# Optimization experiments

Hardware: AMD Instinct MI355X
Metric: run time of the kernel (lower is better)

Reference implementation:

```python
import jax, jax.numpy as jnp
import numpy as np

NX = NY = NZ = 256   # linear_freqs
D1 = D2 = D3 = 8     # reduced_freqs
DF = 16              # feature_dim
NPTS = 131072


def softplus_b10(x):
    # torch F.softplus(x, beta=10, threshold=1)
    bx = 10.0 * x
    return jnp.where(bx > 1.0, x, 0.1 * jnp.log1p(jnp.exp(jnp.minimum(bx, 30.0))))


def grid_sample2d(vol, gx, gy):
    """Bilinear grid_sample, align_corners=True. vol:[C,H,W] (complex ok),
    gx,gy:[N] in [-1,1] (gx indexes W, gy indexes H). Returns [C,N]."""
    C, H, W = vol.shape
    ix = (gx + 1.0) * 0.5 * (W - 1)
    iy = (gy + 1.0) * 0.5 * (H - 1)
    x0f = jnp.floor(ix)
    y0f = jnp.floor(iy)
    wx = ix - x0f
    wy = iy - y0f
    x0 = jnp.clip(x0f.astype(jnp.int32), 0, W - 1)
    x1 = jnp.clip(x0 + 1, 0, W - 1)
    y0 = jnp.clip(y0f.astype(jnp.int32), 0, H - 1)
    y1 = jnp.clip(y0 + 1, 0, H - 1)
    v00 = vol[:, y0, x0]
    v01 = vol[:, y0, x1]
    v10 = vol[:, y1, x0]
    v11 = vol[:, y1, x1]
    return (v00 * (1 - wy) * (1 - wx) + v01 * (1 - wy) * wx
            + v10 * wy * (1 - wx) + v11 * wy * wx)


def batch_irfft(ph, x, ff, T):
    """ph:[D,d,N] complex, x:[N] in [-1,1], ff:[d] freqs. Returns [D,N]."""
    xx = (x + 1.0) * 0.5 * (T - 1) / T                    # [N]
    ang = 2.0 * np.pi * xx[:, None] * ff[None, :]         # [N,d]
    scale = jnp.where(ff > 0, 2.0, 1.0)
    tw_re = jnp.cos(ang) * scale
    tw_im = jnp.sin(ang) * scale
    return (jnp.einsum('dfn,nf->dn', ph.real, tw_re)
            - jnp.einsum('dfn,nf->dn', ph.imag, tw_im))


def setup_inputs() -> dict:
    key = jax.random.key(0)
    ks = jax.random.split(key, 8)
    inputs = jax.random.uniform(ks[0], (NPTS, 3), jnp.float32, minval=-1.0, maxval=1.0)
    s = 0.01
    Fx_re = jax.random.normal(ks[1], (1, DF, D1, NY, NZ), jnp.float32) * s
    Fx_im = jax.random.normal(ks[2], (1, DF, D1, NY, NZ), jnp.float32) * s
    Fy_re = jax.random.normal(ks[3], (1, DF, NX, D2, NZ), jnp.float32) * s
    Fy_im = jax.random.normal(ks[4], (1, DF, NX, D2, NZ), jnp.float32) * s
    Fz_re = jax.random.normal(ks[5], (1, DF, NX, NY, D3), jnp.float32) * s
    Fz_im = jax.random.normal(ks[6], (1, DF, NX, NY, D3), jnp.float32) * s
    alpha_params = jnp.array([0.001], jnp.float32)
    return {"inputs": inputs, "Fx_re": Fx_re, "Fx_im": Fx_im,
            "Fy_re": Fy_re, "Fy_im": Fy_im, "Fz_re": Fz_re, "Fz_im": Fz_im,
            "alpha_params": alpha_params}


def reference(inputs, Fx_re, Fx_im, Fy_re, Fy_im, Fz_re, Fz_im, alpha_params):
    alpha = softplus_b10(alpha_params)[0]
    Fx = (Fx_re + 1j * Fx_im) * alpha        # [1,D,d1,Ny,Nz]
    Fy = (Fy_re + 1j * Fy_im) * alpha        # [1,D,Nx,d2,Nz]
    Fz = (Fz_re + 1j * Fz_im) * alpha        # [1,D,Nx,Ny,d3]
    # inverse FFT over the two full (linear) spectral axes
    Fx = jnp.fft.ifftn(Fx, axes=(3, 4), norm='forward')
    Fy = jnp.fft.ifftn(Fy, axes=(2, 4), norm='forward')
    Fz = jnp.fft.ifftn(Fz, axes=(2, 3), norm='forward')
    xs, ys, zs = inputs[:, 0], inputs[:, 1], inputs[:, 2]
    N = inputs.shape[0]
    kx = jnp.arange(D1, dtype=jnp.float32)   # linear sampling axis [0,1,...]
    ky = jnp.arange(D2, dtype=jnp.float32)
    kz = jnp.arange(D3, dtype=jnp.float32)
    # complex bilinear gathers (H,W) = (Ny,Nz) / (Nx,Nz) / (Ny,Nx)
    fx = grid_sample2d(Fx.reshape(DF * D1, NY, NZ), zs, ys).reshape(DF, D1, N)
    fy = grid_sample2d(jnp.transpose(Fy, (0, 1, 3, 2, 4)).reshape(DF * D2, NX, NZ),
                       zs, xs).reshape(DF, D2, N)
    fz = grid_sample2d(jnp.transpose(Fz, (0, 1, 4, 3, 2)).reshape(DF * D3, NY, NX),
                       xs, ys).reshape(DF, D3, N)
    fxx = batch_irfft(fx, xs, kx, NX)
    fyy = batch_irfft(fy, ys, ky, NY)
    fzz = batch_irfft(fz, zs, kz, NZ)
    return (fxx + fyy + fzz).T               # [N, DF]
```

## Files before the change

kernel.cpp:

```cpp
#include <hip/hip_runtime.h>
#include <hip/hip_fp16.h>
#include <math.h>

#define NPTS 131072
#define RS 264

__device__ __forceinline__ float dev_alpha(const float* __restrict__ ap) {
    float x = ap[0];
    float bx = 10.0f * x;
    if (bx > 1.0f) return x;
    float e = expf(fminf(bx, 30.0f));
    return 0.1f * log1pf(e);
}

__device__ __forceinline__ void fft16_reg(float* re, float* im) {
    #define SW(a,b) { float t=re[a]; re[a]=re[b]; re[b]=t; t=im[a]; im[a]=im[b]; im[b]=t; }
    SW(1,8) SW(2,4) SW(3,12) SW(5,10) SW(7,14) SW(11,13)
    #undef SW
    const float C[8] = {1.f, 0.9238795325112867f, 0.7071067811865476f, 0.3826834323650898f,
                        0.f, -0.3826834323650898f, -0.7071067811865476f, -0.9238795325112867f};
    const float S[8] = {0.f, 0.3826834323650898f, 0.7071067811865476f, 0.9238795325112867f,
                        1.f, 0.9238795325112867f, 0.7071067811865476f, 0.3826834323650898f};
    #pragma unroll
    for (int m = 1; m < 16; m <<= 1) {
        #pragma unroll
        for (int k = 0; k < 16; k += 2 * m) {
            #pragma unroll
            for (int j = 0; j < m; ++j) {
                float wc = C[j * (8 / m)], ws = S[j * (8 / m)];
                int i0 = k + j, i1 = i0 + m;
                float tr = re[i1] * wc - im[i1] * ws;
                float ti = re[i1] * ws + im[i1] * wc;
                re[i1] = re[i0] - tr; im[i1] = im[i0] - ti;
                re[i0] += tr;         im[i0] += ti;
            }
        }
    }
}

__device__ __forceinline__ void fft256_block(float* lre, float* lim, int tid) {
    const int r = tid >> 4, s = tid & 15;
    float xr[16], xi[16];
    #pragma unroll
    for (int a = 0; a < 16; ++a) {
        xr[a] = lre[r * RS + 16 * a + s];
        xi[a] = lim[r * RS + 16 * a + s];
    }
    __syncthreads();
    fft16_reg(xr, xi);
    #pragma unroll
    for (int c = 0; c < 16; ++c) {
        float sn, cs;
        __sincosf(0.0245436926061703f * (float)(s * c), &sn, &cs);
        float tr = xr[c] * cs - xi[c] * sn;
        float ti = xr[c] * sn + xi[c] * cs;
        int idx = r * RS + 16 * c + (s ^ c);
        lre[idx] = tr; lim[idx] = ti;
    }
    __syncthreads();
    #pragma unroll
    for (int b = 0; b < 16; ++b) {
        int idx = r * RS + 16 * s + (b ^ s);
        xr[b] = lre[idx]; xi[b] = lim[idx];
    }
    __syncthreads();
    fft16_reg(xr, xi);
    #pragma unroll
    for (int d = 0; d < 16; ++d) {
        int idx = r * RS + 16 * d + s;
        lre[idx] = xr[d]; lim[idx] = xi[d];
    }
    __syncthreads();
}

__device__ __forceinline__ unsigned packh2(float re, float im) {
    return __builtin_bit_cast(unsigned, __floats2half2_rn(re, im));
}

__global__ __launch_bounds__(256) void fft_pass1_xy(
    const float4* __restrict__ Fre4, const float4* __restrict__ Fim4,
    const float* __restrict__ alpha_p, uint4* __restrict__ GT4,
    int Sd4, int Sa4)
{
    __shared__ float lre[16 * RS], lim[16 * RS];
    const int tid = threadIdx.x, bg = blockIdx.x;
    const int d = bg & 7, ag = (bg >> 3) & 15, f = bg >> 7;
    const int a0 = ag * 16, c = f * 8 + d;
    const int base4 = f * 131072 + d * Sd4 + a0 * Sa4;
    const float alpha = dev_alpha(alpha_p);
    #pragma unroll
    for (int j = 0; j < 4; ++j) {
        int i4 = tid + 256 * j;
        int ar = i4 >> 6, b4 = i4 & 63;
        float4 vr = Fre4[base4 + ar * Sa4 + b4];
        float4 vi = Fim4[base4 + ar * Sa4 + b4];
        int o = ar * RS + 4 * b4;
        lre[o+0]=vr.x*alpha; lre[o+1]=vr.y*alpha; lre[o+2]=vr.z*alpha; lre[o+3]=vr.w*alpha;
        lim[o+0]=vi.x*alpha; lim[o+1]=vi.y*alpha; lim[o+2]=vi.z*alpha; lim[o+3]=vi.w*alpha;
    }
    __syncthreads();
    fft256_block(lre, lim, tid);
    const int g = tid >> 2, rq = tid & 3;
    #pragma unroll
    for (int j = 0; j < 4; ++j) {
        int k = g + 64 * j;
        uint4 ov;
        ov.x = packh2(lre[(4*rq+0)*RS+k], lim[(4*rq+0)*RS+k]);
        ov.y = packh2(lre[(4*rq+1)*RS+k], lim[(4*rq+1)*RS+k]);
        ov.z = packh2(lre[(4*rq+2)*RS+k], lim[(4*rq+2)*RS+k]);
        ov.w = packh2(lre[(4*rq+3)*RS+k], lim[(4*rq+3)*RS+k]);
        GT4[((c * 256 + k) * 256 + a0) / 4 + rq] = ov;
    }
}

__global__ __launch_bounds__(256) void fft_pass2_xy(
    const uint4* __restrict__ GT4, uint4* __restrict__ V4)
{
    __shared__ float lre[16 * RS], lim[16 * RS];
    const int tid = threadIdx.x, bg = blockIdx.x;
    const int cg = bg & 7, b = bg >> 3, c0 = cg * 16;
    #pragma unroll
    for (int j = 0; j < 4; ++j) {
        int i4 = tid + 256 * j;
        int cr = i4 >> 6, a4 = i4 & 63;
        uint4 gv = GT4[(((c0 + cr) * 256 + b) * 256) / 4 + a4];
        int o = cr * RS + 4 * a4;
        float2 e;
        e = __half22float2(__builtin_bit_cast(__half2, gv.x)); lre[o+0]=e.x; lim[o+0]=e.y;
        e = __half22float2(__builtin_bit_cast(__half2, gv.y)); lre[o+1]=e.x; lim[o+1]=e.y;
        e = __half22float2(__builtin_bit_cast(__half2, gv.z)); lre[o+2]=e.x; lim[o+2]=e.y;
        e = __half22float2(__builtin_bit_cast(__half2, gv.w)); lre[o+3]=e.x; lim[o+3]=e.y;
    }
    __syncthreads();
    fft256_block(lre, lim, tid);
    const int g = tid >> 2, cq = tid & 3;
    #pragma unroll
    for (int j = 0; j < 4; ++j) {
        int k = g + 64 * j;
        uint4 ov;
        ov.x = packh2(lre[(4*cq+0)*RS+k], lim[(4*cq+0)*RS+k]);
        ov.y = packh2(lre[(4*cq+1)*RS+k], lim[(4*cq+1)*RS+k]);
        ov.z = packh2(lre[(4*cq+2)*RS+k], lim[(4*cq+2)*RS+k]);
        ov.w = packh2(lre[(4*cq+3)*RS+k], lim[(4*cq+3)*RS+k]);
        V4[((b * 256 + k) * 128 + c0) / 4 + cq] = ov;
    }
}

__global__ __launch_bounds__(256) void fft_pass1_z(
    const float4* __restrict__ Fre4, const float4* __restrict__ Fim4,
    const float* __restrict__ alpha_p, uint4* __restrict__ GTz4)
{
    __shared__ float lre[16 * RS], lim[16 * RS];
    const int tid = threadIdx.x, bg = blockIdx.x;
    const int f = bg >> 7, kxp = bg & 127;
    const int base4 = f * 131072 + kxp * 1024;
    const float alpha = dev_alpha(alpha_p);
    #pragma unroll
    for (int j = 0; j < 4; ++j) {
        int i4 = tid + 256 * j;
        int kxo = i4 >> 9, ky = (i4 & 511) >> 1, t0 = i4 & 1;
        float4 vr = Fre4[base4 + i4];
        float4 vi = Fim4[base4 + i4];
        int row = kxo * 8 + 4 * t0;
        lre[(row+0)*RS + ky] = vr.x*alpha; lim[(row+0)*RS + ky] = vi.x*alpha;
        lre[(row+1)*RS + ky] = vr.y*alpha; lim[(row+1)*RS + ky] = vi.y*alpha;
        lre[(row+2)*RS + ky] = vr.z*alpha; lim[(row+2)*RS + ky] = vi.z*alpha;
        lre[(row+3)*RS + ky] = vr.w*alpha; lim[(row+3)*RS + ky] = vi.w*alpha;
    }
    __syncthreads();
    fft256_block(lre, lim, tid);
    const int g = tid >> 2, rq = tid & 3;
    #pragma unroll
    for (int j = 0; j < 4; ++j) {
        int k = g + 64 * j;
        uint4 ov;
        ov.x = packh2(lre[(4*rq+0)*RS+k], lim[(4*rq+0)*RS+k]);
        ov.y = packh2(lre[(4*rq+1)*RS+k], lim[(4*rq+1)*RS+k]);
        ov.z = packh2(lre[(4*rq+2)*RS+k], lim[(4*rq+2)*RS+k]);
        ov.w = packh2(lre[(4*rq+3)*RS+k], lim[(4*rq+3)*RS+k]);
        GTz4[k * 8192 + f * 512 + kxp * 4 + rq] = ov;
    }
}

__global__ __launch_bounds__(256) void fft_pass2_z(
    const uint4* __restrict__ GTz4, uint4* __restrict__ V4)
{
    __shared__ float lre[16 * RS], lim[16 * RS];
    const int tid = threadIdx.x, bg = blockIdx.x;
    const int fp = bg & 7, b = bg >> 3;
    const int base4 = b * 8192 + fp * 1024;
    #pragma unroll
    for (int j = 0; j < 4; ++j) {
        int i4 = tid + 256 * j;
        int fo = i4 >> 9, kx = (i4 & 511) >> 1, t0 = i4 & 1;
        uint4 gv = GTz4[base4 + i4];
        int row = fo * 8 + 4 * t0;
        float2 e;
        e = __half22float2(__builtin_bit_cast(__half2, gv.x)); lre[(row+0)*RS+kx]=e.x; lim[(row+0)*RS+kx]=e.y;
        e = __half22float2(__builtin_bit_cast(__half2, gv.y)); lre[(row+1)*RS+kx]=e.x; lim[(row+1)*RS+kx]=e.y;
        e = __half22float2(__builtin_bit_cast(__half2, gv.z)); lre[(row+2)*RS+kx]=e.x; lim[(row+2)*RS+kx]=e.y;
        e = __half22float2(__builtin_bit_cast(__half2, gv.w)); lre[(row+3)*RS+kx]=e.x; lim[(row+3)*RS+kx]=e.y;
    }
    __syncthreads();
    fft256_block(lre, lim, tid);
    const int g = tid >> 2, rq = tid & 3;
    #pragma unroll
    for (int j = 0; j < 4; ++j) {
        int k = g + 64 * j;
        uint4 ov;
        ov.x = packh2(lre[(4*rq+0)*RS+k], lim[(4*rq+0)*RS+k]);
        ov.y = packh2(lre[(4*rq+1)*RS+k], lim[(4*rq+1)*RS+k]);
        ov.z = packh2(lre[(4*rq+2)*RS+k], lim[(4*rq+2)*RS+k]);
        ov.w = packh2(lre[(4*rq+3)*RS+k], lim[(4*rq+3)*RS+k]);
        V4[(b * 256 + k) * 32 + fp * 4 + rq] = ov;
    }
}

__device__ __forceinline__ int bin8(float v) {
    return min(max((int)((v + 1.0f) * 127.5f), 0), 255);
}
__global__ __launch_bounds__(256) void zero_hist(unsigned* __restrict__ h) {
    h[blockIdx.x * 256 + threadIdx.x] = 0;
}
__global__ __launch_bounds__(256) void hist_k(const float* __restrict__ pts, unsigned* __restrict__ h) {
    int pid = blockIdx.x * 256 + threadIdx.x;
    int key = bin8(pts[pid * 3 + 2]) * 256 + bin8(pts[pid * 3 + 1]);
    atomicAdd(&h[key], 1u);
}
__global__ __launch_bounds__(256) void scan_k(const unsigned* __restrict__ h, unsigned* __restrict__ cur) {
    __shared__ unsigned part[256];
    const int t = threadIdx.x;
    unsigned sum = 0;
    for (int i = 0; i < 256; ++i) sum += h[t * 256 + i];
    part[t] = sum;
    __syncthreads();
    for (int o = 1; o < 256; o <<= 1) {
        unsigned v = part[t];
        unsigned add = (t >= o) ? part[t - o] : 0u;
        __syncthreads();
        part[t] = v + add;
        __syncthreads();
    }
    unsigned run = (t > 0) ? part[t - 1] : 0u;
    for (int i = 0; i < 256; ++i) {
        cur[t * 256 + i] = run;
        run += h[t * 256 + i];
    }
}
__global__ __launch_bounds__(256) void scatter_k(const float* __restrict__ pts,
                                                 unsigned* __restrict__ cur,
                                                 float4* __restrict__ ptsS) {
    int pid = blockIdx.x * 256 + threadIdx.x;
    float x = pts[pid * 3 + 0], y = pts[pid * 3 + 1], z = pts[pid * 3 + 2];
    int key = bin8(z) * 256 + bin8(y);
    unsigned pos = atomicAdd(&cur[key], 1u);
    ptsS[pos] = make_float4(x, y, z, __uint_as_float((unsigned)pid));
}

__device__ __forceinline__ float4 bsample(const uint2* __restrict__ V,
                                          float gx, float gy, bool swap, int lane) {
    float ix = (gx + 1.0f) * 127.5f;
    float iy = (gy + 1.0f) * 127.5f;
    float x0f = floorf(ix), y0f = floorf(iy);
    float wx = ix - x0f, wy = iy - y0f;
    int x0 = min(max((int)x0f, 0), 255);
    int x1 = min(x0 + 1, 255);
    int y0 = min(max((int)y0f, 0), 255);
    int y1 = min(y0 + 1, 255);
    int rA, rB, rC, rD;
    if (swap) { rA = y0*256+x0; rB = y0*256+x1; rC = y1*256+x0; rD = y1*256+x1; }
    else      { rA = x0*256+y0; rB = x1*256+y0; rC = x0*256+y1; rD = x1*256+y1; }
    uint2 a = V[rA * 64 + lane];
    uint2 b = V[rB * 64 + lane];
    uint2 c = V[rC * 64 + lane];
    uint2 d = V[rD * 64 + lane];
    __half2 w00 = __float2half2_rn((1.0f - wy) * (1.0f - wx));
    __half2 w01 = __float2half2_rn((1.0f - wy) * wx);
    __half2 w10 = __float2half2_rn(wy * (1.0f - wx));
    __half2 w11 = __float2half2_rn(wy * wx);
    __half2 acc0 = __hmul2(w00, __builtin_bit_cast(__half2, a.x));
    __half2 acc1 = __hmul2(w00, __builtin_bit_cast(__half2, a.y));
    acc0 = __hfma2(w01, __builtin_bit_cast(__half2, b.x), acc0);
    acc1 = __hfma2(w01, __builtin_bit_cast(__half2, b.y), acc1);
    acc0 = __hfma2(w10, __builtin_bit_cast(__half2, c.x), acc0);
    acc1 = __hfma2(w10, __builtin_bit_cast(__half2, c.y), acc1);
    acc0 = __hfma2(w11, __builtin_bit_cast(__half2, d.x), acc0);
    acc1 = __hfma2(w11, __builtin_bit_cast(__half2, d.y), acc1);
    return make_float4(__low2float(acc0), __high2float(acc0),
                       __low2float(acc1), __high2float(acc1));
}

__device__ __forceinline__ float irdft(float4 s, float tw, int lane) {
    const float TWO_PI = 6.28318530717958647692f;
    float xx = (tw + 1.0f) * 0.5f * (255.0f / 256.0f);
    int k0 = (lane & 3) * 2;
    float sa, ca, sb, cb;
    __sincosf(TWO_PI * xx * (float)k0,       &sa, &ca);
    __sincosf(TWO_PI * xx * (float)(k0 + 1), &sb, &cb);
    float sc0 = (k0 > 0) ? 2.0f : 1.0f;
    return sc0 * (s.x * ca - s.y * sa) + 2.0f * (s.z * cb - s.w * sb);
}

__global__ __launch_bounds__(256) void sample_all(
    const uint2* __restrict__ Vx, const uint2* __restrict__ Vy, const uint2* __restrict__ Vz,
    const float4* __restrict__ ptsS, float* __restrict__ out)
{
    const int lb = blockIdx.x;
    const int chunk = (lb & 7) * 4096 + (lb >> 3);
    const int wid = chunk * 4 + ((int)threadIdx.x >> 6);
    const int lane = threadIdx.x & 63;
    float4 p = ptsS[wid];
    const float xs = p.x, ys = p.y, zs = p.z;
    const int pid = (int)__float_as_uint(p.w);

    float4 sx = bsample(Vx, zs, ys, false, lane);
    float4 sy = bsample(Vy, zs, xs, false, lane);
    float4 sz = bsample(Vz, xs, ys, true, lane);

    float pv = irdft(sx, xs, lane) + irdft(sy, ys, lane) + irdft(sz, zs, lane);
    pv += __shfl_xor(pv, 1, 64);
    pv += __shfl_xor(pv, 2, 64);
    if ((lane & 3) == 0) out[pid * 16 + (lane >> 2)] = pv;
}

extern "C" void kernel_launch(void* const* d_in, const int* in_sizes, int n_in,
                              void* d_out, int out_size, void* d_ws, size_t ws_size,
                              hipStream_t stream) {
    const float* pts     = (const float*)d_in[0];
    const float* Fx_re   = (const float*)d_in[1];
    const float* Fx_im   = (const float*)d_in[2];
    const float* Fy_re   = (const float*)d_in[3];
    const float* Fy_im   = (const float*)d_in[4];
    const float* Fz_re   = (const float*)d_in[5];
    const float* Fz_im   = (const float*)d_in[6];
    const float* alpha_p = (const float*)d_in[7];
    float* out = (float*)d_out;

    char* ws = (char*)d_ws;
    const size_t MB = 1024 * 1024;
    uint4* Vx4 = (uint4*)(ws);
    uint4* Vy4 = (uint4*)(ws + 32 * MB);
    uint4* Vz4 = (uint4*)(ws + 64 * MB);
    uint4* GT4 = (uint4*)(ws + 96 * MB);
    unsigned* hist = (unsigned*)(ws + 96 * MB);
    unsigned* cur  = (unsigned*)(ws + 96 * MB + 256 * 1024);
    float4*   ptsS = (float4*)  (ws + 96 * MB + 512 * 1024);

    fft_pass1_xy<<<2048, 256, 0, stream>>>((const float4*)Fx_re, (const float4*)Fx_im, alpha_p, GT4, 16384, 64);
    fft_pass2_xy<<<2048, 256, 0, stream>>>(GT4, Vx4);
    fft_pass1_xy<<<2048, 256, 0, stream>>>((const float4*)Fy_re, (const float4*)Fy_im, alpha_p, GT4, 64, 512);
    fft_pass2_xy<<<2048, 256, 0, stream>>>(GT4, Vy4);
    fft_pass1_z<<<2048, 256, 0, stream>>>((const float4*)Fz_re, (const float4*)Fz_im, alpha_p, GT4);
    fft_pass2_z<<<2048, 256, 0, stream>>>(GT4, Vz4);

    zero_hist<<<256, 256, 0, stream>>>(hist);
    hist_k<<<NPTS / 256, 256, 0, stream>>>(pts, hist);
    scan_k<<<1, 256, 0, stream>>>(hist, cur);
    scatter_k<<<NPTS / 256, 256, 0, stream>>>(pts, cur, ptsS);

    sample_all<<<NPTS / 4, 256, 0, stream>>>((const uint2*)Vx4, (const uint2*)Vy4, (const uint2*)Vz4,
                                             ptsS, out);
}
```

Before: 384.0 us.

## Batch FFT passes across all three planes and widen sampler loads

Merges the six FFT launches into two batched kernels, one per pass, each covering all three planes, with separate transpose buffers when the workspace is large enough. A fallback path keeps sequential launches. FFT blocks shrink to 128 threads working on 8 rows, and results are packed to half2 inside shared memory before store. The sampler now uses 32 lanes per point with uint4 gathers and computes the twiddles by recurrence. The aim is fewer launches, better occupancy and fewer gather instructions, at the cost of more workspace and a different rounding path.

Result: no change. 391.5 us (+2.0%).

```diff
diff --git a/kernel.cpp b/kernel.cpp
--- a/kernel.cpp
+++ b/kernel.cpp
@@ -12,6 +12,8 @@
     float e = expf(fminf(bx, 30.0f));
     return 0.1f * log1pf(e);
 }
+
+__device__ __forceinline__ __half2 bch(unsigned u) { return __builtin_bit_cast(__half2, u); }
 
 __device__ __forceinline__ void fft16_reg(float* re, float* im) {
     #define SW(a,b) { float t=re[a]; re[a]=re[b]; re[b]=t; t=im[a]; im[a]=im[b]; im[b]=t; }
@@ -38,7 +40,7 @@
     }
 }
 
-__device__ __forceinline__ void fft256_block(float* lre, float* lim, int tid) {
+__device__ __forceinline__ void fft256_block8(float* lre, float* lim, int tid) {
     const int r = tid >> 4, s = tid & 15;
     float xr[16], xi[16];
     #pragma unroll
@@ -65,155 +67,190 @@
     }
     __syncthreads();
     fft16_reg(xr, xi);
-    #pragma unroll
-    for (int d = 0; d < 16; ++d) {
-        int idx = r * RS + 16 * d + s;
-        lre[idx] = xr[d]; lim[idx] = xi[d];
-    }
-    __syncthreads();
-}
-
-__device__ __forceinline__ unsigned packh2(float re, float im) {
-    return __builtin_bit_cast(unsigned, __floats2half2_rn(re, im));
-}
-
-__global__ __launch_bounds__(256) void fft_pass1_xy(
-    const float4* __restrict__ Fre4, const float4* __restrict__ Fim4,
-    const float* __restrict__ alpha_p, uint4* __restrict__ GT4,
-    int Sd4, int Sa4)
-{
-    __shared__ float lre[16 * RS], lim[16 * RS];
-    const int tid = threadIdx.x, bg = blockIdx.x;
-    const int d = bg & 7, ag = (bg >> 3) & 15, f = bg >> 7;
-    const int a0 = ag * 16, c = f * 8 + d;
+    __half2* hb = (__half2*)lre;
+    #pragma unroll
+    for (int d = 0; d < 16; ++d)
+        hb[r * RS + 16 * d + s] = __floats2half2_rn(xr[d], xi[d]);
+    __syncthreads();
+}
+
+__device__ __forceinline__ void dev_p1_xy(int bg, const float4* __restrict__ Fre4,
+        const float4* __restrict__ Fim4, float alpha, uint4* __restrict__ GT4,
+        int Sd4, int Sa4, float* lre, float* lim, int tid)
+{
+    const int d = bg & 7, ag = (bg >> 3) & 31, f = bg >> 8;
+    const int a0 = ag * 8, c = f * 8 + d;
     const int base4 = f * 131072 + d * Sd4 + a0 * Sa4;
-    const float alpha = dev_alpha(alpha_p);
-    #pragma unroll
-    for (int j = 0; j < 4; ++j) {
-        int i4 = tid + 256 * j;
+    #pragma unroll
+    for (int j = 0; j < 4; ++j) {
+        int i4 = tid + 128 * j;
         int ar = i4 >> 6, b4 = i4 & 63;
         float4 vr = Fre4[base4 + ar * Sa4 + b4];
         float4 vi = Fim4[base4 + ar * Sa4 + b4];
         int o = ar * RS + 4 * b4;
-        lre[o+0]=vr.x*alpha; lre[o+1]=vr.y*alpha; lre[o+2]=vr.z*alpha; lre[o+3]=vr.w*alpha;
-        lim[o+0]=vi.x*alpha; lim[o+1]=vi.y*alpha; lim[o+2]=vi.z*alpha; lim[o+3]=vi.w*alpha;
-    }
-    __syncthreads();
-    fft256_block(lre, lim, tid);
-    const int g = tid >> 2, rq = tid & 3;
+        *(float4*)&lre[o] = make_float4(vr.x*alpha, vr.y*alpha, vr.z*alpha, vr.w*alpha);
+        *(float4*)&lim[o] = make_float4(vi.x*alpha, vi.y*alpha, vi.z*alpha, vi.w*alpha);
+    }
+    __syncthreads();
+    fft256_block8(lre, lim, tid);
+    const unsigned* hw = (const unsigned*)lre;
+    const int g = tid >> 1, rq = tid & 1;
     #pragma unroll
     for (int j = 0; j < 4; ++j) {
         int k = g + 64 * j;
-        uint4 ov;
-        ov.x = packh2(lre[(4*rq+0)*RS+k], lim[(4*rq+0)*RS+k]);
-        ov.y = packh2(lre[(4*rq+1)*RS+k], lim[(4*rq+1)*RS+k]);
-        ov.z = packh2(lre[(4*rq+2)*RS+k], lim[(4*rq+2)*RS+k]);
-        ov.w = packh2(lre[(4*rq+3)*RS+k], lim[(4*rq+3)*RS+k]);
-        GT4[((c * 256 + k) * 256 + a0) / 4 + rq] = ov;
-    }
-}
-
-__global__ __launch_bounds__(256) void fft_pass2_xy(
-    const uint4* __restrict__ GT4, uint4* __restrict__ V4)
-{
-    __shared__ float lre[16 * RS], lim[16 * RS];
-    const int tid = threadIdx.x, bg = blockIdx.x;
-    const int cg = bg & 7, b = bg >> 3, c0 = cg * 16;
-    #pragma unroll
-    for (int j = 0; j < 4; ++j) {
-        int i4 = tid + 256 * j;
+        uint4 ov = make_uint4(hw[(4*rq+0)*RS + k], hw[(4*rq+1)*RS + k],
+                              hw[(4*rq+2)*RS + k], hw[(4*rq+3)*RS + k]);
+        GT4[c * 16384 + k * 64 + ag * 2 + rq] = ov;
+    }
+}
+
+__device__ __forceinline__ void dev_p2_xy(int bg, const uint4* __restrict__ GT4,
+        uint4* __restrict__ V4, float* lre, float* lim, int tid)
+{
+    const int cg = bg & 15, b = bg >> 4, c0 = cg * 8;
+    #pragma unroll
+    for (int j = 0; j < 4; ++j) {
+        int i4 = tid + 128 * j;
         int cr = i4 >> 6, a4 = i4 & 63;
-        uint4 gv = GT4[(((c0 + cr) * 256 + b) * 256) / 4 + a4];
+        uint4 gv = GT4[(c0 + cr) * 16384 + b * 64 + a4];
         int o = cr * RS + 4 * a4;
         float2 e;
-        e = __half22float2(__builtin_bit_cast(__half2, gv.x)); lre[o+0]=e.x; lim[o+0]=e.y;
-        e = __half22float2(__builtin_bit_cast(__half2, gv.y)); lre[o+1]=e.x; lim[o+1]=e.y;
-        e = __half22float2(__builtin_bit_cast(__half2, gv.z)); lre[o+2]=e.x; lim[o+2]=e.y;
-        e = __half22float2(__builtin_bit_cast(__half2, gv.w)); lre[o+3]=e.x; lim[o+3]=e.y;
-    }
-    __syncthreads();
-    fft256_block(lre, lim, tid);
-    const int g = tid >> 2, cq = tid & 3;
+        e = __half22float2(bch(gv.x)); lre[o+0]=e.x; lim[o+0]=e.y;
+        e = __half22float2(bch(gv.y)); lre[o+1]=e.x; lim[o+1]=e.y;
+        e = __half22float2(bch(gv.z)); lre[o+2]=e.x; lim[o+2]=e.y;
+        e = __half22float2(bch(gv.w)); lre[o+3]=e.x; lim[o+3]=e.y;
+    }
+    __syncthreads();
+    fft256_block8(lre, lim, tid);
+    const unsigned* hw = (const unsigned*)lre;
+    const int g = tid >> 1, rq = tid & 1;
     #pragma unroll
     for (int j = 0; j < 4; ++j) {
         int k = g + 64 * j;
-        uint4 ov;
-        ov.x = packh2(lre[(4*cq+0)*RS+k], lim[(4*cq+0)*RS+k]);
-        ov.y = packh2(lre[(4*cq+1)*RS+k], lim[(4*cq+1)*RS+k]);
-        ov.z = packh2(lre[(4*cq+2)*RS+k], lim[(4*cq+2)*RS+k]);
-        ov.w = packh2(lre[(4*cq+3)*RS+k], lim[(4*cq+3)*RS+k]);
-        V4[((b * 256 + k) * 128 + c0) / 4 + cq] = ov;
-    }
-}
-
-__global__ __launch_bounds__(256) void fft_pass1_z(
+        uint4 ov = make_uint4(hw[(4*rq+0)*RS + k], hw[(4*rq+1)*RS + k],
+                              hw[(4*rq+2)*RS + k], hw[(4*rq+3)*RS + k]);
+        V4[(b * 256 + k) * 32 + cg * 2 + rq] = ov;
+    }
+}
+
+__device__ __forceinline__ void dev_p1_z(int bg, const float4* __restrict__ Fre4,
+        const float4* __restrict__ Fim4, float alpha, uint4* __restrict__ GTz4,
+        float* lre, float* lim, int tid)
+{
+    const int f = bg >> 8, kx = bg & 255;
+    const int base4 = f * 131072 + kx * 512;
+    #pragma unroll
+    for (int j = 0; j < 4; ++j) {
+        int i4 = tid + 128 * j;
+        int ky = i4 >> 1, t0 = i4 & 1;
+        float4 vr = Fre4[base4 + i4];
+        float4 vi = Fim4[base4 + i4];
+        int r0 = 4 * t0;
+        lre[(r0+0)*RS + ky] = vr.x*alpha; lim[(r0+0)*RS + ky] = vi.x*alpha;
+        lre[(r0+1)*RS + ky] = vr.y*alpha; lim[(r0+1)*RS + ky] = vi.y*alpha;
+        lre[(r0+2)*RS + ky] = vr.z*alpha; lim[(r0+2)*RS + ky] = vi.z*alpha;
+        lre[(r0+3)*RS + ky] = vr.w*alpha; lim[(r0+3)*RS + ky] = vi.w*alpha;
+    }
+    __syncthreads();
+    fft256_block8(lre, lim, tid);
+    const unsigned* hw = (const unsigned*)lre;
+    const int g = tid >> 1, rq = tid & 1;
+    #pragma unroll
+    for (int j = 0; j < 4; ++j) {
+        int k = g + 64 * j;
+        uint4 ov = make_uint4(hw[(4*rq+0)*RS + k], hw[(4*rq+1)*RS + k],
+                              hw[(4*rq+2)*RS + k], hw[(4*rq+3)*RS + k]);
+        GTz4[k * 8192 + f * 512 + kx * 2 + rq] = ov;
+    }
+}
+
+__device__ __forceinline__ void dev_p2_z(int bg, const uint4* __restrict__ GTz4,
+        uint4* __restrict__ V4, float* lre, float* lim, int tid)
+{
+    const int fg = bg & 15, b = bg >> 4;
+    const int base4 = b * 8192 + fg * 512;
+    #pragma unroll
+    for (int j = 0; j < 4; ++j) {
+        int i4 = tid + 128 * j;
+        int kx = i4 >> 1, t0 = i4 & 1;
+        uint4 gv = GTz4[base4 + i4];
+        int r0 = 4 * t0;
+        float2 e;
+        e = __half22float2(bch(gv.x)); lre[(r0+0)*RS + kx]=e.x; lim[(r0+0)*RS + kx]=e.y;
+        e = __half22float2(bch(gv.y)); lre[(r0+1)*RS + kx]=e.x; lim[(r0+1)*RS + kx]=e.y;
+        e = __half22float2(bch(gv.z)); lre[(r0+2)*RS + kx]=e.x; lim[(r0+2)*RS + kx]=e.y;
+        e = __half22float2(bch(gv.w)); lre[(r0+3)*RS + kx]=e.x; lim[(r0+3)*RS + kx]=e.y;
+    }
+    __syncthreads();
+    fft256_block8(lre, lim, tid);
+    const unsigned* hw = (const unsigned*)lre;
+    const int g = tid >> 1, rq = tid & 1;
+    #pragma unroll
+    for (int j = 0; j < 4; ++j) {
+        int k = g + 64 * j;
+        uint4 ov = make_uint4(hw[(4*rq+0)*RS + k], hw[(4*rq+1)*RS + k],
+                              hw[(4*rq+2)*RS + k], hw[(4*rq+3)*RS + k]);
+        V4[(b * 256 + k) * 32 + fg * 2 + rq] = ov;
+    }
+}
+
+__global__ __launch_bounds__(128) void fft_pass1_all(
+    const float4* __restrict__ Fxr, const float4* __restrict__ Fxi,
+    const float4* __restrict__ Fyr, const float4* __restrict__ Fyi,
+    const float4* __restrict__ Fzr, const float4* __restrict__ Fzi,
+    const float* __restrict__ alpha_p,
+    uint4* __restrict__ GTx, uint4* __restrict__ GTy, uint4* __restrict__ GTz)
+{
+    __shared__ __align__(16) float lre[8 * RS];
+    __shared__ __align__(16) float lim[8 * RS];
+    const int tid = threadIdx.x, bg = blockIdx.x;
+    const float alpha = dev_alpha(alpha_p);
+    if (bg < 4096)       dev_p1_xy(bg,        Fxr, Fxi, alpha, GTx, 16384, 64,  lre, lim, tid);
+    else if (bg < 8192)  dev_p1_xy(bg - 4096, Fyr, Fyi, alpha, GTy, 64,    512, lre, lim, tid);
+    else                 dev_p1_z (bg - 8192, Fzr, Fzi, alpha, GTz,            lre, lim, tid);
+}
+
+__global__ __launch_bounds__(128) void fft_pass2_all(
+    const uint4* __restrict__ GTx, const uint4* __restrict__ GTy, const uint4* __restrict__ GTz,
+    uint4* __restrict__ Vx, uint4* __restrict__ Vy, uint4* __restrict__ Vz)
+{
+    __shared__ __align__(16) float lre[8 * RS];
+    __shared__ __align__(16) float lim[8 * RS];
+    const int tid = threadIdx.x, bg = blockIdx.x;
+    if (bg < 4096)       dev_p2_xy(bg,        GTx, Vx, lre, lim, tid);
+    else if (bg < 8192)  dev_p2_xy(bg - 4096, GTy, Vy, lre, lim, tid);
+    else                 dev_p2_z (bg - 8192, GTz, Vz, lre, lim, tid);
+}
+
+__global__ __launch_bounds__(128) void fft_p1xy_k(
+    const float4* __restrict__ Fre4, const float4* __restrict__ Fim4,
+    const float* __restrict__ alpha_p, uint4* __restrict__ GT4, int Sd4, int Sa4)
+{
+    __shared__ __align__(16) float lre[8 * RS];
+    __shared__ __align__(16) float lim[8 * RS];
+    dev_p1_xy(blockIdx.x, Fre4, Fim4, dev_alpha(alpha_p), GT4, Sd4, Sa4, lre, lim, threadIdx.x);
+}
+__global__ __launch_bounds__(128) void fft_p2xy_k(
+    const uint4* __restrict__ GT4, uint4* __restrict__ V4)
+{
+    __shared__ __align__(16) float lre[8 * RS];
+    __shared__ __align__(16) float lim[8 * RS];
+    dev_p2_xy(blockIdx.x, GT4, V4, lre, lim, threadIdx.x);
+}
+__global__ __launch_bounds__(128) void fft_p1z_k(
     const float4* __restrict__ Fre4, const float4* __restrict__ Fim4,
     const float* __restrict__ alpha_p, uint4* __restrict__ GTz4)
 {
-    __shared__ float lre[16 * RS], lim[16 * RS];
-    const int tid = threadIdx.x, bg = blockIdx.x;
-    const int f = bg >> 7, kxp = bg & 127;
-    const int base4 = f * 131072 + kxp * 1024;
-    const float alpha = dev_alpha(alpha_p);
-    #pragma unroll
-    for (int j = 0; j < 4; ++j) {
-        int i4 = tid + 256 * j;
-        int kxo = i4 >> 9, ky = (i4 & 511) >> 1, t0 = i4 & 1;
-        float4 vr = Fre4[base4 + i4];
-        float4 vi = Fim4[base4 + i4];
-        int row = kxo * 8 + 4 * t0;
-        lre[(row+0)*RS + ky] = vr.x*alpha; lim[(row+0)*RS + ky] = vi.x*alpha;
-        lre[(row+1)*RS + ky] = vr.y*alpha; lim[(row+1)*RS + ky] = vi.y*alpha;
-        lre[(row+2)*RS + ky] = vr.z*alpha; lim[(row+2)*RS + ky] = vi.z*alpha;
-        lre[(row+3)*RS + ky] = vr.w*alpha; lim[(row+3)*RS + ky] = vi.w*alpha;
-    }
-    __syncthreads();
-    fft256_block(lre, lim, tid);
-    const int g = tid >> 2, rq = tid & 3;
-    #pragma unroll
-    for (int j = 0; j < 4; ++j) {
-        int k = g + 64 * j;
-        uint4 ov;
-        ov.x = packh2(lre[(4*rq+0)*RS+k], lim[(4*rq+0)*RS+k]);
-        ov.y = packh2(lre[(4*rq+1)*RS+k], lim[(4*rq+1)*RS+k]);
-        ov.z = packh2(lre[(4*rq+2)*RS+k], lim[(4*rq+2)*RS+k]);
-        ov.w = packh2(lre[(4*rq+3)*RS+k], lim[(4*rq+3)*RS+k]);
-        GTz4[k * 8192 + f * 512 + kxp * 4 + rq] = ov;
-    }
-}
-
-__global__ __launch_bounds__(256) void fft_pass2_z(
+    __shared__ __align__(16) float lre[8 * RS];
+    __shared__ __align__(16) float lim[8 * RS];
+    dev_p1_z(blockIdx.x, Fre4, Fim4, dev_alpha(alpha_p), GTz4, lre, lim, threadIdx.x);
+}
+__global__ __launch_bounds__(128) void fft_p2z_k(
     const uint4* __restrict__ GTz4, uint4* __restrict__ V4)
 {
-    __shared__ float lre[16 * RS], lim[16 * RS];
-    const int tid = threadIdx.x, bg = blockIdx.x;
-    const int fp = bg & 7, b = bg >> 3;
-    const int base4 = b * 8192 + fp * 1024;
-    #pragma unroll
-    for (int j = 0; j < 4; ++j) {
-        int i4 = tid + 256 * j;
-        int fo = i4 >> 9, kx = (i4 & 511) >> 1, t0 = i4 & 1;
-        uint4 gv = GTz4[base4 + i4];
-        int row = fo * 8 + 4 * t0;
-        float2 e;
-        e = __half22float2(__builtin_bit_cast(__half2, gv.x)); lre[(row+0)*RS+kx]=e.x; lim[(row+0)*RS+kx]=e.y;
-        e = __half22float2(__builtin_bit_cast(__half2, gv.y)); lre[(row+1)*RS+kx]=e.x; lim[(row+1)*RS+kx]=e.y;
-        e = __half22float2(__builtin_bit_cast(__half2, gv.z)); lre[(row+2)*RS+kx]=e.x; lim[(row+2)*RS+kx]=e.y;
-        e = __half22float2(__builtin_bit_cast(__half2, gv.w)); lre[(row+3)*RS+kx]=e.x; lim[(row+3)*RS+kx]=e.y;
-    }
-    __syncthreads();
-    fft256_block(lre, lim, tid);
-    const int g = tid >> 2, rq = tid & 3;
-    #pragma unroll
-    for (int j = 0; j < 4; ++j) {
-        int k = g + 64 * j;
-        uint4 ov;
-        ov.x = packh2(lre[(4*rq+0)*RS+k], lim[(4*rq+0)*RS+k]);
-        ov.y = packh2(lre[(4*rq+1)*RS+k], lim[(4*rq+1)*RS+k]);
-        ov.z = packh2(lre[(4*rq+2)*RS+k], lim[(4*rq+2)*RS+k]);
-        ov.w = packh2(lre[(4*rq+3)*RS+k], lim[(4*rq+3)*RS+k]);
-        V4[(b * 256 + k) * 32 + fp * 4 + rq] = ov;
-    }
+    __shared__ __align__(16) float lre[8 * RS];
+    __shared__ __align__(16) float lim[8 * RS];
+    dev_p2_z(blockIdx.x, GTz4, V4, lre, lim, threadIdx.x);
 }
 
 __device__ __forceinline__ int bin8(float v) {
@@ -257,8 +294,9 @@
     ptsS[pos] = make_float4(x, y, z, __uint_as_float((unsigned)pid));
 }
 
-__device__ __forceinline__ float4 bsample(const uint2* __restrict__ V,
-                                          float gx, float gy, bool swap, int lane) {
+__device__ __forceinline__ void bsample4(const uint4* __restrict__ V,
+        float gx, float gy, bool swap, int L, float* re, float* im)
+{
     float ix = (gx + 1.0f) * 127.5f;
     float iy = (gy + 1.0f) * 127.5f;
     float x0f = floorf(ix), y0f = floorf(iy);
@@ -270,69 +308,84 @@
     int rA, rB, rC, rD;
     if (swap) { rA = y0*256+x0; rB = y0*256+x1; rC = y1*256+x0; rD = y1*256+x1; }
     else      { rA = x0*256+y0; rB = x1*256+y0; rC = x0*256+y1; rD = x1*256+y1; }
-    uint2 a = V[rA * 64 + lane];
-    uint2 b = V[rB * 64 + lane];
-    uint2 c = V[rC * 64 + lane];
-    uint2 d = V[rD * 64 + lane];
+    uint4 A = V[rA * 32 + L];
+    uint4 B = V[rB * 32 + L];
+    uint4 C = V[rC * 32 + L];
+    uint4 D = V[rD * 32 + L];
     __half2 w00 = __float2half2_rn((1.0f - wy) * (1.0f - wx));
     __half2 w01 = __float2half2_rn((1.0f - wy) * wx);
     __half2 w10 = __float2half2_rn(wy * (1.0f - wx));
     __half2 w11 = __float2half2_rn(wy * wx);
-    __half2 acc0 = __hmul2(w00, __builtin_bit_cast(__half2, a.x));
-    __half2 acc1 = __hmul2(w00, __builtin_bit_cast(__half2, a.y));
-    acc0 = __hfma2(w01, __builtin_bit_cast(__half2, b.x), acc0);
-    acc1 = __hfma2(w01, __builtin_bit_cast(__half2, b.y), acc1);
-    acc0 = __hfma2(w10, __builtin_bit_cast(__half2, c.x), acc0);
-    acc1 = __hfma2(w10, __builtin_bit_cast(__half2, c.y), acc1);
-    acc0 = __hfma2(w11, __builtin_bit_cast(__half2, d.x), acc0);
-    acc1 = __hfma2(w11, __builtin_bit_cast(__half2, d.y), acc1);
-    return make_float4(__low2float(acc0), __high2float(acc0),
-                       __low2float(acc1), __high2float(acc1));
-}
-
-__device__ __forceinline__ float irdft(float4 s, float tw, int lane) {
+    __half2 a0 = __hmul2(w00, bch(A.x)), a1 = __hmul2(w00, bch(A.y));
+    __half2 a2 = __hmul2(w00, bch(A.z)), a3 = __hmul2(w00, bch(A.w));
+    a0 = __hfma2(w01, bch(B.x), a0); a1 = __hfma2(w01, bch(B.y), a1);
+    a2 = __hfma2(w01, bch(B.z), a2); a3 = __hfma2(w01, bch(B.w), a3);
+    a0 = __hfma2(w10, bch(C.x), a0); a1 = __hfma2(w10, bch(C.y), a1);
+    a2 = __hfma2(w10, bch(C.z), a2); a3 = __hfma2(w10, bch(C.w), a3);
+    a0 = __hfma2(w11, bch(D.x), a0); a1 = __hfma2(w11, bch(D.y), a1);
+    a2 = __hfma2(w11, bch(D.z), a2); a3 = __hfma2(w11, bch(D.w), a3);
+    float2 e;
+    e = __half22float2(a0); re[0] = e.x; im[0] = e.y;
+    e = __half22float2(a1); re[1] = e.x; im[1] = e.y;
+    e = __half22float2(a2); re[2] = e.x; im[2] = e.y;
+    e = __half22float2(a3); re[3] = e.x; im[3] = e.y;
+}
+
+__device__ __forceinline__ float irdft4(const float* re, const float* im, float tw, int L)
+{
     const float TWO_PI = 6.28318530717958647692f;
     float xx = (tw + 1.0f) * 0.5f * (255.0f / 256.0f);
-    int k0 = (lane & 3) * 2;
-    float sa, ca, sb, cb;
-    __sincosf(TWO_PI * xx * (float)k0,       &sa, &ca);
-    __sincosf(TWO_PI * xx * (float)(k0 + 1), &sb, &cb);
-    float sc0 = (k0 > 0) ? 2.0f : 1.0f;
-    return sc0 * (s.x * ca - s.y * sa) + 2.0f * (s.z * cb - s.w * sb);
+    float th = TWO_PI * xx;
+    int d0 = (L & 1) * 4;
+    float s0, c0, st, ct;
+    __sincosf(th * (float)d0, &s0, &c0);
+    __sincosf(th, &st, &ct);
+    float c = c0, s = s0;
+    float p = 0.f;
+    #pragma unroll
+    for (int i = 0; i < 4; ++i) {
+        p += 2.0f * (re[i] * c - im[i] * s);
+        float cn = c * ct - s * st;
+        s = s * ct + c * st;
+        c = cn;
+    }
+    if (d0 == 0) p -= re[0];
+    return p;
 }
 
 __global__ __launch_bounds__(256) void sample_all(
-    const uint2* __restrict__ Vx, const uint2* __restrict__ Vy, const uint2* __restrict__ Vz,
+    const uint4* __restrict__ Vx, const uint4* __restrict__ Vy, const uint4* __restrict__ Vz,
     const float4* __restrict__ ptsS, float* __restrict__ out)
 {
     const int lb = blockIdx.x;
-    const int chunk = (lb & 7) * 4096 + (lb >> 3);
-    const int wid = chunk * 4 + ((int)threadIdx.x >> 6);
-    const int lane = threadIdx.x & 63;
+    const int chunk = (lb & 7) * 2048 + (lb >> 3);
+    const int tid = threadIdx.x;
+    const int L = tid & 31;
+    const int wid = chunk * 8 + (tid >> 5);
     float4 p = ptsS[wid];
     const float xs = p.x, ys = p.y, zs = p.z;
     const int pid = (int)__float_as_uint(p.w);
 
-    float4 sx = bsample(Vx, zs, ys, false, lane);
-    float4 sy = bsample(Vy, zs, xs, false, lane);
-    float4 sz = bsample(Vz, xs, ys, true, lane);
-
-    float pv = irdft(sx, xs, lane) + irdft(sy, ys, lane) + irdft(sz, zs, lane);
+    float rex[4], imx[4], rey[4], imy[4], rez[4], imz[4];
+    bsample4(Vx, zs, ys, false, L, rex, imx);
+    bsample4(Vy, zs, xs, false, L, rey, imy);
+    bsample4(Vz, xs, ys, true,  L, rez, imz);
+
+    float pv = irdft4(rex, imx, xs, L) + irdft4(rey, imy, ys, L) + irdft4(rez, imz, zs, L);
     pv += __shfl_xor(pv, 1, 64);
-    pv += __shfl_xor(pv, 2, 64);
-    if ((lane & 3) == 0) out[pid * 16 + (lane >> 2)] = pv;
+    if ((L & 1) == 0) out[pid * 16 + (L >> 1)] = pv;
 }
 
 extern "C" void kernel_launch(void* const* d_in, const int* in_sizes, int n_in,
                               void* d_out, int out_size, void* d_ws, size_t ws_size,
                               hipStream_t stream) {
     const float* pts     = (const float*)d_in[0];
-    const float* Fx_re   = (const float*)d_in[1];
-    const float* Fx_im   = (const float*)d_in[2];
-    const float* Fy_re   = (const float*)d_in[3];
-    const float* Fy_im   = (const float*)d_in[4];
-    const float* Fz_re   = (const float*)d_in[5];
-    const float* Fz_im   = (const float*)d_in[6];
+    const float4* Fxr    = (const float4*)d_in[1];
+    const float4* Fxi    = (const float4*)d_in[2];
+    const float4* Fyr    = (const float4*)d_in[3];
+    const float4* Fyi    = (const float4*)d_in[4];
+    const float4* Fzr    = (const float4*)d_in[5];
+    const float4* Fzi    = (const float4*)d_in[6];
     const float* alpha_p = (const float*)d_in[7];
     float* out = (float*)d_out;
 
@@ -341,23 +394,34 @@
     uint4* Vx4 = (uint4*)(ws);
     uint4* Vy4 = (uint4*)(ws + 32 * MB);
     uint4* Vz4 = (uint4*)(ws + 64 * MB);
-    uint4* GT4 = (uint4*)(ws + 96 * MB);
-    unsigned* hist = (unsigned*)(ws + 96 * MB);
-    unsigned* cur  = (unsigned*)(ws + 96 * MB + 256 * 1024);
-    float4*   ptsS = (float4*)  (ws + 96 * MB + 512 * 1024);
-
-    fft_pass1_xy<<<2048, 256, 0, stream>>>((const float4*)Fx_re, (const float4*)Fx_im, alpha_p, GT4, 16384, 64);
-    fft_pass2_xy<<<2048, 256, 0, stream>>>(GT4, Vx4);
-    fft_pass1_xy<<<2048, 256, 0, stream>>>((const float4*)Fy_re, (const float4*)Fy_im, alpha_p, GT4, 64, 512);
-    fft_pass2_xy<<<2048, 256, 0, stream>>>(GT4, Vy4);
-    fft_pass1_z<<<2048, 256, 0, stream>>>((const float4*)Fz_re, (const float4*)Fz_im, alpha_p, GT4);
-    fft_pass2_z<<<2048, 256, 0, stream>>>(GT4, Vz4);
-
+
+    size_t sortoff;
+    if (ws_size >= (size_t)195 * MB) {
+        uint4* GTx = (uint4*)(ws + 96 * MB);
+        uint4* GTy = (uint4*)(ws + 128 * MB);
+        uint4* GTz = (uint4*)(ws + 160 * MB);
+        sortoff = 192 * MB;
+        fft_pass1_all<<<12288, 128, 0, stream>>>(Fxr, Fxi, Fyr, Fyi, Fzr, Fzi, alpha_p,
+                                                 GTx, GTy, GTz);
+        fft_pass2_all<<<12288, 128, 0, stream>>>(GTx, GTy, GTz, Vx4, Vy4, Vz4);
+    } else {
+        uint4* GT = (uint4*)(ws + 96 * MB);
+        sortoff = 96 * MB;
+        fft_p1xy_k<<<4096, 128, 0, stream>>>(Fxr, Fxi, alpha_p, GT, 16384, 64);
+        fft_p2xy_k<<<4096, 128, 0, stream>>>(GT, Vx4);
+        fft_p1xy_k<<<4096, 128, 0, stream>>>(Fyr, Fyi, alpha_p, GT, 64, 512);
+        fft_p2xy_k<<<4096, 128, 0, stream>>>(GT, Vy4);
+        fft_p1z_k<<<4096, 128, 0, stream>>>(Fzr, Fzi, alpha_p, GT);
+        fft_p2z_k<<<4096, 128, 0, stream>>>(GT, Vz4);
+    }
+
+    unsigned* hist = (unsigned*)(ws + sortoff);
+    unsigned* cur  = (unsigned*)(ws + sortoff + 256 * 1024);
+    float4*   ptsS = (float4*)  (ws + sortoff + 512 * 1024);
     zero_hist<<<256, 256, 0, stream>>>(hist);
     hist_k<<<NPTS / 256, 256, 0, stream>>>(pts, hist);
     scan_k<<<1, 256, 0, stream>>>(hist, cur);
     scatter_k<<<NPTS / 256, 256, 0, stream>>>(pts, cur, ptsS);
 
-    sample_all<<<NPTS / 4, 256, 0, stream>>>((const uint2*)Vx4, (const uint2*)Vy4, (const uint2*)Vz4,
-                                             ptsS, out);
-}
+    sample_all<<<16384, 256, 0, stream>>>(Vx4, Vy4, Vz4, ptsS, out);
+}
```
